# Performance work log

Hardware: AMD Instinct MI355X
Metric: run time of the kernel (lower is better)

## Reference

```python
import jax, jax.numpy as jnp
import numpy as np

S_MUL, V_MUL = 32, 16          # 32x0e + 16x1o
NODE_DIM = S_MUL + 3 * V_MUL   # 80
LATENT = 128
INV_SQRT3 = 1.0 / np.sqrt(3.0)          # wigner 3j (1,1,0) / (0,1,1) / (1,0,1) factor
C_SCALAR = np.float32(1.0 / np.sqrt(48.0))   # path_norm 'element': fan into 0e = 32*1 + 16*1
C_VECTOR = np.float32(np.sqrt(3.0 / 48.0))   # irrep dim 3 / fan 48 for 1o output


def setup_inputs() -> dict:
    rng = np.random.default_rng(0)
    B, n_atoms, radius = 2048, 32, 5.0
    N = B * n_atoms
    # atoms uniform in a 10A cube -> ~300 edges per 32-atom graph at r=5
    pos_g = rng.uniform(0.0, 10.0, size=(B, n_atoms, 3)).astype(np.float32)
    diff = pos_g[:, :, None, :] - pos_g[:, None, :, :]
    d2 = (diff * diff).sum(-1)
    mask = (d2 <= radius * radius) & (d2 > 0.0)   # same predicate as build_radius_graph
    b_idx, i_idx, j_idx = np.nonzero(mask)
    edge_index = np.stack([b_idx * n_atoms + i_idx, b_idx * n_atoms + j_idx]).astype(np.int32)
    pos = pos_g.reshape(N, 3)
    z = rng.integers(0, 100, size=N).astype(np.int32)
    batch = np.repeat(np.arange(B, dtype=np.int32), n_atoms)
    L = 3  # num_layers

    def w(*shape, scale=1.0):
        return jnp.asarray((rng.standard_normal(shape) * scale).astype(np.float32))

    return dict(
        pos=jnp.asarray(pos), z=jnp.asarray(z), batch=jnp.asarray(batch),
        edge_index=jnp.asarray(edge_index), num_graphs=B,
        emb=w(100, S_MUL),                      # nn.Embedding(100, 32) ~ N(0,1)
        W_s2n=w(S_MUL, S_MUL),                  # e3nn Linear 32x0e -> 32x0e path
        W1=w(L, S_MUL, S_MUL),                  # tp path 0e x 0e -> 0e
        W2=w(L, S_MUL, V_MUL),                  # tp path 0e x 1o -> 1o
        W3=w(L, V_MUL, V_MUL),                  # tp path 1o x 0e -> 1o
        W4=w(L, V_MUL, S_MUL),                  # tp path 1o x 1o -> 0e
        Ws=w(L, S_MUL, S_MUL),                  # e3nn Linear scalar block
        Wv=w(L, V_MUL, V_MUL),                  # e3nn Linear vector block
        Wr1=w(NODE_DIM, 256, scale=1.0 / np.sqrt(NODE_DIM)), br1=jnp.zeros((256,), jnp.float32),
        Wr2=w(256, LATENT, scale=1.0 / np.sqrt(256.0)), br2=jnp.zeros((LATENT,), jnp.float32),
    )


def _forward(pos, emb, W_s2n, W1, W2, W3, W4, Ws, Wv, Wr1, br1, Wr2, br2,
             z, batch, edge_index, num_graphs):
    N = pos.shape[0]
    src, dst = edge_index[0], edge_index[1]
    # atom embedding -> node irreps (only 0e->0e path exists; vectors start at 0)
    s = (emb[z] @ W_s2n) * np.float32(1.0 / np.sqrt(S_MUL))   # (N, 32)
    v = jnp.zeros((N, V_MUL, 3), pos.dtype)                   # (N, 16, 3)
    # spherical harmonics, normalize=True, 'component': Y0 = 1, Y1 = sqrt(3) * r_hat
    rij = pos[dst] - pos[src]                                 # (E, 3)
    sh1 = np.float32(np.sqrt(3.0)) * rij / jnp.linalg.norm(rij, axis=-1, keepdims=True)
    for l in range(W1.shape[0]):
        ss, vs = s[src], v[src]                               # gather (E,32), (E,16,3)
        # FullyConnectedTensorProduct(node, sh, node), uvw weights, sh0 == 1
        m_s = C_SCALAR * (jnp.einsum('eu,uw->ew', ss, W1[l])
                          + INV_SQRT3 * jnp.einsum('eui,ei,uw->ew', vs, sh1, W4[l]))
        m_v = (C_VECTOR * INV_SQRT3) * (jnp.einsum('eu,ei,uw->ewi', ss, sh1, W2[l])
                                        + jnp.einsum('eui,uw->ewi', vs, W3[l]))
        a_s = jax.ops.segment_sum(m_s, dst, num_segments=N)   # index_add_ scatter
        a_v = jax.ops.segment_sum(m_v, dst, num_segments=N)
        # e3nn Linear (per-irrep block, 1/sqrt(fan_in)) then relu on FULL feature (as in source)
        h_s = jax.nn.relu((a_s @ Ws[l]) * np.float32(1.0 / np.sqrt(S_MUL)))
        h_v = jax.nn.relu(jnp.einsum('nvi,vw->nwi', a_v, Wv[l]) * np.float32(1.0 / np.sqrt(V_MUL)))
        s, v = s + h_s, v + h_v                               # residual
    x = jnp.concatenate([s, v.reshape(N, V_MUL * 3)], axis=-1)  # (N, 80)
    hg = jax.ops.segment_sum(x, batch, num_segments=num_graphs) # sum-pool per graph
    return jax.nn.relu(hg @ Wr1 + br1) @ Wr2 + br2              # (B, latent)


def reference(pos, emb, W_s2n, W1, W2, W3, W4, Ws, Wv, Wr1, br1, Wr2, br2,
              z, batch, edge_index, num_graphs):
    return _forward(pos, emb, W_s2n, W1, W2, W3, W4, Ws, Wv, Wr1, br1, Wr2, br2,
                    z, batch, edge_index, num_graphs)
```

## Files before the change

### kernel.cpp

```cpp
#include <hip/hip_runtime.h>
#include <math.h>

typedef __attribute__((ext_vector_type(8))) short bf16x8;
typedef __attribute__((ext_vector_type(4))) float f32x4;

#define SQRT3F     1.7320508075688772f
#define SCALE_T    0.17677669529663687f
#define SCALE_M1   0.025515518153991442f
#define SCALE_M2   0.014731391274719739f
#define SCALE_M34  0.036084391824351615f

#define FSTR 40
#define ASTR 72

__device__ __forceinline__ ushort f2bf(float f) {
    union { float f; unsigned u; } v; v.f = f;
    unsigned u = v.u;
    return (ushort)((u + 0x7FFFu + ((u >> 16) & 1u)) >> 16);
}
__device__ __forceinline__ float bf2f(ushort h) {
    union { unsigned u; float f; } v; v.u = ((unsigned)h) << 16;
    return v.f;
}
__device__ __forceinline__ f32x4 mfma(bf16x8 a, bf16x8 b, f32x4 c) {
    return __builtin_amdgcn_mfma_f32_16x16x32_bf16(a, b, c, 0, 0, 0);
}
__device__ __forceinline__ void storeAgg(ushort* AG, f32x4 t, int u0, int n) {
    uint2 u;
    u.x = f2bf(t[0]) | ((unsigned)f2bf(t[1]) << 16);
    u.y = f2bf(t[2]) | ((unsigned)f2bf(t[3]) << 16);
    *(uint2*)&AG[n*ASTR + u0] = u;
}

__global__ void prep_kernel(const float* __restrict__ pos,
                            const float* __restrict__ emb,
                            const float* __restrict__ W_s2n,
                            const float* __restrict__ W1, const float* __restrict__ W2,
                            const float* __restrict__ W3, const float* __restrict__ W4,
                            const float* __restrict__ Ws, const float* __restrict__ Wv,
                            ushort* __restrict__ adjF, ushort* __restrict__ Tbf,
                            ushort* __restrict__ Mbf, int NG)
{
    int idx = blockIdx.x * blockDim.x + threadIdx.x;
    const int NA = NG * 2 * 64;
    if (idx < NA) {
        int g = idx >> 7, r = idx & 127, nt = r >> 6, l = r & 63;
        int nl = nt*16 + (l & 15);
        int k0 = (l >> 4) * 8;
        int ng = g*32 + nl;
        float px = pos[3*ng], py = pos[3*ng+1], pz = pos[3*ng+2];
        ushort o0[8], o1[8], o2[8], o3[8];
        #pragma unroll
        for (int jj = 0; jj < 8; ++jj) {
            int j = g*32 + k0 + jj;
            float dx = __fsub_rn(px, pos[3*j]);
            float dy = __fsub_rn(py, pos[3*j+1]);
            float dz = __fsub_rn(pz, pos[3*j+2]);
            float d2 = __fadd_rn(__fadd_rn(__fmul_rn(dx,dx), __fmul_rn(dy,dy)),
                                 __fmul_rn(dz,dz));
            bool on = (d2 <= 25.0f) && (d2 > 0.0f);
            float rinv = on ? rsqrtf(d2) * SQRT3F : 0.f;
            o0[jj] = on ? f2bf(1.0f) : 0;
            o1[jj] = f2bf(dx * rinv);
            o2[jj] = f2bf(dy * rinv);
            o3[jj] = f2bf(dz * rinv);
        }
        const ushort* srcs[4] = {o0, o1, o2, o3};
        #pragma unroll
        for (int w = 0; w < 4; ++w) {
            const ushort* s = srcs[w];
            uint4 u;
            u.x = s[0] | ((unsigned)s[1] << 16);
            u.y = s[2] | ((unsigned)s[3] << 16);
            u.z = s[4] | ((unsigned)s[5] << 16);
            u.w = s[6] | ((unsigned)s[7] << 16);
            *(uint4*)(adjF + (((size_t)(g*4 + w)*2 + nt)*64 + l)*8) = u;
        }
        return;
    }
    idx -= NA;
    if (idx < 3200) {
        int r = idx >> 5, c = idx & 31;
        float acc = 0.f;
        for (int k = 0; k < 32; ++k) acc += emb[r*32 + k] * W_s2n[k*32 + c];
        Tbf[idx] = f2bf(acc * SCALE_T);
        return;
    }
    idx -= 3200;
    if (idx < 3*48*64) {
        int lyr = idx / 3072, rem = idx % 3072;
        int row = rem >> 6, u = rem & 63;
        float val = 0.f;
        if (row < 32) {
            int w = row;
            if (u < 32) {
                float a = 0.f;
                for (int k = 0; k < 32; ++k)
                    a += W1[lyr*1024 + u*32 + k] * Ws[lyr*1024 + k*32 + w];
                val = a * SCALE_M1;
            } else if (u < 48) {
                int uu = u - 32; float a = 0.f;
                for (int k = 0; k < 32; ++k)
                    a += W4[lyr*512 + uu*32 + k] * Ws[lyr*1024 + k*32 + w];
                val = a * SCALE_M2;
            }
        } else {
            int w = row - 32;
            if (u < 32) {
                float a = 0.f;
                for (int k = 0; k < 16; ++k)
                    a += W2[lyr*512 + u*16 + k] * Wv[lyr*256 + k*16 + w];
                val = a * SCALE_M34;
            } else if (u < 48) {
                int uu = u - 32; float a = 0.f;
                for (int k = 0; k < 16; ++k)
                    a += W3[lyr*256 + uu*16 + k] * Wv[lyr*256 + k*16 + w];
                val = a * SCALE_M34;
            }
        }
        Mbf[lyr*3072 + row*64 + u] = f2bf(val);
    }
}

__global__ __launch_bounds__(256)
void gnn_kernel(const ushort* __restrict__ Tbf, const int* __restrict__ z,
                const ushort* __restrict__ adjF, const ushort* __restrict__ Mbf,
                float* __restrict__ hg, int B)
{
    __shared__ ushort lM[3*48*ASTR];
    __shared__ ushort feat[4][80*FSTR];
    __shared__ ushort agg[4][32*ASTR];

    const int tid = threadIdx.x;
    for (int i = tid; i < 3*48*8; i += 256) {
        int row = i >> 3, u0 = (i & 7) * 8;
        uint4 m = *(const uint4*)(Mbf + row*64 + u0);
        uint2 a; a.x = m.x; a.y = m.y;
        uint2 b; b.x = m.z; b.y = m.w;
        *(uint2*)&lM[row*ASTR + u0]     = a;
        *(uint2*)&lM[row*ASTR + u0 + 4] = b;
    }
    const int wv = tid >> 6, l = tid & 63;
    const int g  = blockIdx.x*4 + wv;
    ushort* F  = feat[wv];
    ushort* AG = agg[wv];

    for (int i = l; i < 32*(ASTR/2); i += 64) ((uint*)AG)[i] = 0;
    for (int i = l; i < 48*(FSTR/2); i += 64) ((uint*)(F + 32*FSTR))[i] = 0;
    {
        int n = l & 31, h = l >> 5;
        int zg = z[g*32 + n];
        uint4 t0 = *(const uint4*)(Tbf + zg*32 + h*16);
        uint4 t1 = *(const uint4*)(Tbf + zg*32 + h*16 + 8);
        unsigned ua[8] = {t0.x, t0.y, t0.z, t0.w, t1.x, t1.y, t1.z, t1.w};
        #pragma unroll
        for (int q = 0; q < 8; ++q) {
            F[(h*16 + 2*q    )*FSTR + n] = (ushort)ua[q];
            F[(h*16 + 2*q + 1)*FSTR + n] = (ushort)(ua[q] >> 16);
        }
    }
    bf16x8 adjf[4][2];
    #pragma unroll
    for (int w = 0; w < 4; ++w)
        #pragma unroll
        for (int nt = 0; nt < 2; ++nt)
            adjf[w][nt] = *(const bf16x8*)(adjF + (((size_t)(g*4 + w)*2 + nt)*64 + l)*8);
    __syncthreads();

    const int ln = l & 15, kq = l >> 4;
    const f32x4 z4 = {0.f, 0.f, 0.f, 0.f};

    for (int lay = 0; lay < 3; ++lay) {
        const ushort* Msl = lM + lay*48*ASTR;
        bf16x8 fs0 = *(const bf16x8*)&F[(     ln)*FSTR + kq*8];
        bf16x8 fs1 = *(const bf16x8*)&F[(16 + ln)*FSTR + kq*8];
        bf16x8 fv0 = *(const bf16x8*)&F[(32 + ln)*FSTR + kq*8];
        bf16x8 fv1 = *(const bf16x8*)&F[(48 + ln)*FSTR + kq*8];
        bf16x8 fv2 = *(const bf16x8*)&F[(64 + ln)*FSTR + kq*8];

        #pragma unroll
        for (int nt = 0; nt < 2; ++nt) {
            f32x4 t;
            t = mfma(fs0, adjf[0][nt], z4);
            storeAgg(AG, t,      kq*4, nt*16 + ln);
            t = mfma(fs1, adjf[0][nt], z4);
            storeAgg(AG, t, 16 + kq*4, nt*16 + ln);
            t = mfma(fv2, adjf[3][nt], z4);
            t = mfma(fv1, adjf[2][nt], t);
            t = mfma(fv0, adjf[1][nt], t);
            storeAgg(AG, t, 32 + kq*4, nt*16 + ln);
        }
        f32x4 hs[2][2] = {{z4, z4}, {z4, z4}};
        #pragma unroll
        for (int kc = 0; kc < 2; ++kc) {
            bf16x8 m0 = *(const bf16x8*)&Msl[(     ln)*ASTR + kc*32 + kq*8];
            bf16x8 m1 = *(const bf16x8*)&Msl[(16 + ln)*ASTR + kc*32 + kq*8];
            #pragma unroll
            for (int nt = 0; nt < 2; ++nt) {
                bf16x8 bg = *(const bf16x8*)&AG[(nt*16 + ln)*ASTR + kc*32 + kq*8];
                hs[0][nt] = mfma(m0, bg, hs[0][nt]);
                hs[1][nt] = mfma(m1, bg, hs[1][nt]);
            }
        }
        #pragma unroll
        for (int mt = 0; mt < 2; ++mt)
            #pragma unroll
            for (int nt = 0; nt < 2; ++nt) {
                int n = nt*16 + ln;
                #pragma unroll
                for (int r = 0; r < 4; ++r) {
                    int c = mt*16 + kq*4 + r;
                    ushort* p = &F[c*FSTR + n];
                    *p = f2bf(bf2f(*p) + fmaxf(hs[mt][nt][r], 0.f));
                }
            }

        #pragma unroll
        for (int i = 0; i < 3; ++i) {
            bf16x8 fvi = (i == 0) ? fv0 : (i == 1) ? fv1 : fv2;
            #pragma unroll
            for (int nt = 0; nt < 2; ++nt) {
                f32x4 t;
                t = mfma(fs0, adjf[1+i][nt], z4);
                storeAgg(AG, t,      kq*4, nt*16 + ln);
                t = mfma(fs1, adjf[1+i][nt], z4);
                storeAgg(AG, t, 16 + kq*4, nt*16 + ln);
                t = mfma(fvi, adjf[0][nt], z4);
                storeAgg(AG, t, 32 + kq*4, nt*16 + ln);
            }
            f32x4 hv[2] = {z4, z4};
            #pragma unroll
            for (int kc = 0; kc < 2; ++kc) {
                bf16x8 mv = *(const bf16x8*)&Msl[(32 + ln)*ASTR + kc*32 + kq*8];
                #pragma unroll
                for (int nt = 0; nt < 2; ++nt) {
                    bf16x8 bg = *(const bf16x8*)&AG[(nt*16 + ln)*ASTR + kc*32 + kq*8];
                    hv[nt] = mfma(mv, bg, hv[nt]);
                }
            }
            #pragma unroll
            for (int nt = 0; nt < 2; ++nt) {
                int n = nt*16 + ln;
                #pragma unroll
                for (int r = 0; r < 4; ++r) {
                    int c = 32 + i*16 + kq*4 + r;
                    ushort* p = &F[c*FSTR + n];
                    *p = f2bf(bf2f(*p) + fmaxf(hv[nt][r], 0.f));
                }
            }
        }
    }

    for (int f = l; f < 80; f += 64) {
        const ushort* row;
        if (f < 32) row = &F[f*FSTR];
        else { int c = f - 32, w = c/3, i = c - 3*w; row = &F[(32 + i*16 + w)*FSTR]; }
        const uint* r32 = (const uint*)row;
        float acc = 0.f;
        #pragma unroll
        for (int q = 0; q < 16; ++q) {
            uint u = r32[q];
            acc += bf2f((ushort)u) + bf2f((ushort)(u >> 16));
        }
        hg[(size_t)g*80 + f] = acc;
    }
}

__launch_bounds__(256)
__global__ void mlp_kernel(const float* __restrict__ hg,
                           const float* __restrict__ Wr1, const float* __restrict__ br1,
                           const float* __restrict__ Wr2, const float* __restrict__ br2,
                           float* __restrict__ out, int B)
{
    __shared__ __align__(16) float h1[4][256];
    __shared__ float red[4][128];
    const int g0 = blockIdx.x * 4;
    const int w = threadIdx.x;

    float acc0 = br1[w];
    float acc1 = acc0, acc2 = acc0, acc3 = acc0;
    #pragma unroll 4
    for (int f = 0; f < 80; ++f) {
        float wv = Wr1[f*256 + w];
        acc0 = fmaf(hg[(size_t)(g0+0)*80 + f], wv, acc0);
        acc1 = fmaf(hg[(size_t)(g0+1)*80 + f], wv, acc1);
        acc2 = fmaf(hg[(size_t)(g0+2)*80 + f], wv, acc2);
        acc3 = fmaf(hg[(size_t)(g0+3)*80 + f], wv, acc3);
    }
    h1[0][w] = fmaxf(acc0, 0.f);
    h1[1][w] = fmaxf(acc1, 0.f);
    h1[2][w] = fmaxf(acc2, 0.f);
    h1[3][w] = fmaxf(acc3, 0.f);
    __syncthreads();

    const int w2 = threadIdx.x & 127, kh = threadIdx.x >> 7;
    const float4* h1v = (const float4*)(&h1[0][0]);
    float s0 = 0.f, s1 = 0.f, s2 = 0.f, s3 = 0.f;
    #pragma unroll 2
    for (int k4 = kh*32; k4 < kh*32 + 32; ++k4) {
        float4 hA = h1v[0*64 + k4];
        float4 hB = h1v[1*64 + k4];
        float4 hC = h1v[2*64 + k4];
        float4 hD = h1v[3*64 + k4];
        int k = k4 * 4;
        float m0 = Wr2[(size_t)(k+0)*128 + w2];
        float m1 = Wr2[(size_t)(k+1)*128 + w2];
        float m2 = Wr2[(size_t)(k+2)*128 + w2];
        float m3 = Wr2[(size_t)(k+3)*128 + w2];
        s0 = fmaf(hA.x,m0, fmaf(hA.y,m1, fmaf(hA.z,m2, fmaf(hA.w,m3, s0))));
        s1 = fmaf(hB.x,m0, fmaf(hB.y,m1, fmaf(hB.z,m2, fmaf(hB.w,m3, s1))));
        s2 = fmaf(hC.x,m0, fmaf(hC.y,m1, fmaf(hC.z,m2, fmaf(hC.w,m3, s2))));
        s3 = fmaf(hD.x,m0, fmaf(hD.y,m1, fmaf(hD.z,m2, fmaf(hD.w,m3, s3))));
    }
    if (kh) {
        red[0][w2] = s0; red[1][w2] = s1; red[2][w2] = s2; red[3][w2] = s3;
    }
    __syncthreads();
    if (!kh) {
        float b = br2[w2];
        out[(size_t)(g0+0)*128 + w2] = s0 + red[0][w2] + b;
        out[(size_t)(g0+1)*128 + w2] = s1 + red[1][w2] + b;
        out[(size_t)(g0+2)*128 + w2] = s2 + red[2][w2] + b;
        out[(size_t)(g0+3)*128 + w2] = s3 + red[3][w2] + b;
    }
}

extern "C" void kernel_launch(void* const* d_in, const int* in_sizes, int n_in,
                              void* d_out, int out_size, void* d_ws, size_t ws_size,
                              hipStream_t stream)
{
    const float* pos   = (const float*)d_in[0];
    const int*   z     = (const int*)d_in[1];
    const float* emb   = (const float*)d_in[5];
    const float* W_s2n = (const float*)d_in[6];
    const float* W1    = (const float*)d_in[7];
    const float* W2    = (const float*)d_in[8];
    const float* W3    = (const float*)d_in[9];
    const float* W4    = (const float*)d_in[10];
    const float* Ws    = (const float*)d_in[11];
    const float* Wv    = (const float*)d_in[12];
    const float* Wr1   = (const float*)d_in[13];
    const float* br1   = (const float*)d_in[14];
    const float* Wr2   = (const float*)d_in[15];
    const float* br2   = (const float*)d_in[16];
    float* out = (float*)d_out;

    const int B = out_size / 128;
    const int NG = B;

    char* p = (char*)d_ws;
    ushort* adjF = (ushort*)p;  p += (size_t)NG * 4 * 2 * 64 * 8 * 2;
    ushort* Tbf  = (ushort*)p;  p += ((3200*2 + 15) & ~15);
    ushort* Mbf  = (ushort*)p;  p += ((3*48*64*2 + 15) & ~15);
    float*  hg   = (float*)p;   p += (size_t)B * 80 * 4;

    const int prep_total = NG*2*64 + 3200 + 3*48*64;
    prep_kernel<<<(prep_total + 255) / 256, 256, 0, stream>>>(
        pos, emb, W_s2n, W1, W2, W3, W4, Ws, Wv, adjF, Tbf, Mbf, NG);

    gnn_kernel<<<B / 4, 256, 0, stream>>>(Tbf, z, adjF, Mbf, hg, B);

    mlp_kernel<<<B / 4, 256, 0, stream>>>(hg, Wr1, br1, Wr2, br2, out, B);
}
```

Before: 125.9 us.

## Fuse prep, GNN and MLP kernels into a single launch

Merges the three kernels into one. Each block now builds the folded weight matrices, embeddings and adjacency fragments in registers or shared memory itself, and runs the readout MLP on its four graphs from shared memory. This removes two launches and the global round trips for adjF, Tbf, Mbf and hg. In exchange every block recomputes the 3x48x64 weight products and the embedding matmuls, which is redundant work across 512 blocks, and shared memory use grows to about 66KB.

```diff
diff --git a/kernel.cpp b/kernel.cpp
--- a/kernel.cpp
+++ b/kernel.cpp
@@ -32,62 +32,27 @@
     *(uint2*)&AG[n*ASTR + u0] = u;
 }
 
-__global__ void prep_kernel(const float* __restrict__ pos,
-                            const float* __restrict__ emb,
-                            const float* __restrict__ W_s2n,
-                            const float* __restrict__ W1, const float* __restrict__ W2,
-                            const float* __restrict__ W3, const float* __restrict__ W4,
-                            const float* __restrict__ Ws, const float* __restrict__ Wv,
-                            ushort* __restrict__ adjF, ushort* __restrict__ Tbf,
-                            ushort* __restrict__ Mbf, int NG)
+__global__ __launch_bounds__(256)
+void gnn_kernel(const float* __restrict__ pos, const int* __restrict__ z,
+                const float* __restrict__ emb, const float* __restrict__ W_s2n,
+                const float* __restrict__ W1, const float* __restrict__ W2,
+                const float* __restrict__ W3, const float* __restrict__ W4,
+                const float* __restrict__ Ws, const float* __restrict__ Wv,
+                const float* __restrict__ Wr1, const float* __restrict__ br1,
+                const float* __restrict__ Wr2, const float* __restrict__ br2,
+                float* __restrict__ out, int B)
 {
-    int idx = blockIdx.x * blockDim.x + threadIdx.x;
-    const int NA = NG * 2 * 64;
-    if (idx < NA) {
-        int g = idx >> 7, r = idx & 127, nt = r >> 6, l = r & 63;
-        int nl = nt*16 + (l & 15);
-        int k0 = (l >> 4) * 8;
-        int ng = g*32 + nl;
-        float px = pos[3*ng], py = pos[3*ng+1], pz = pos[3*ng+2];
-        ushort o0[8], o1[8], o2[8], o3[8];
-        #pragma unroll
-        for (int jj = 0; jj < 8; ++jj) {
-            int j = g*32 + k0 + jj;
-            float dx = __fsub_rn(px, pos[3*j]);
-            float dy = __fsub_rn(py, pos[3*j+1]);
-            float dz = __fsub_rn(pz, pos[3*j+2]);
-            float d2 = __fadd_rn(__fadd_rn(__fmul_rn(dx,dx), __fmul_rn(dy,dy)),
-                                 __fmul_rn(dz,dz));
-            bool on = (d2 <= 25.0f) && (d2 > 0.0f);
-            float rinv = on ? rsqrtf(d2) * SQRT3F : 0.f;
-            o0[jj] = on ? f2bf(1.0f) : 0;
-            o1[jj] = f2bf(dx * rinv);
-            o2[jj] = f2bf(dy * rinv);
-            o3[jj] = f2bf(dz * rinv);
-        }
-        const ushort* srcs[4] = {o0, o1, o2, o3};
-        #pragma unroll
-        for (int w = 0; w < 4; ++w) {
-            const ushort* s = srcs[w];
-            uint4 u;
-            u.x = s[0] | ((unsigned)s[1] << 16);
-            u.y = s[2] | ((unsigned)s[3] << 16);
-            u.z = s[4] | ((unsigned)s[5] << 16);
-            u.w = s[6] | ((unsigned)s[7] << 16);
-            *(uint4*)(adjF + (((size_t)(g*4 + w)*2 + nt)*64 + l)*8) = u;
-        }
-        return;
-    }
-    idx -= NA;
-    if (idx < 3200) {
-        int r = idx >> 5, c = idx & 31;
-        float acc = 0.f;
-        for (int k = 0; k < 32; ++k) acc += emb[r*32 + k] * W_s2n[k*32 + c];
-        Tbf[idx] = f2bf(acc * SCALE_T);
-        return;
-    }
-    idx -= 3200;
-    if (idx < 3*48*64) {
+    __shared__ __align__(16) char smem[66048];
+    ushort* lM    = (ushort*)smem;
+    ushort* featA = (ushort*)(smem + 20736);
+    ushort* aggA  = (ushort*)(smem + 46336);
+    float*  hgl   = (float*)(smem + 64768);
+    float*  h1    = (float*)aggA;
+    float*  red   = ((float*)aggA) + 1024;
+
+    const int tid = threadIdx.x;
+
+    for (int idx = tid; idx < 3*48*64; idx += 256) {
         int lyr = idx / 3072, rem = idx % 3072;
         int row = rem >> 6, u = rem & 63;
         float val = 0.f;
@@ -118,56 +83,59 @@
                 val = a * SCALE_M34;
             }
         }
-        Mbf[lyr*3072 + row*64 + u] = f2bf(val);
-    }
-}
-
-__global__ __launch_bounds__(256)
-void gnn_kernel(const ushort* __restrict__ Tbf, const int* __restrict__ z,
-                const ushort* __restrict__ adjF, const ushort* __restrict__ Mbf,
-                float* __restrict__ hg, int B)
-{
-    __shared__ ushort lM[3*48*ASTR];
-    __shared__ ushort feat[4][80*FSTR];
-    __shared__ ushort agg[4][32*ASTR];
-
-    const int tid = threadIdx.x;
-    for (int i = tid; i < 3*48*8; i += 256) {
-        int row = i >> 3, u0 = (i & 7) * 8;
-        uint4 m = *(const uint4*)(Mbf + row*64 + u0);
-        uint2 a; a.x = m.x; a.y = m.y;
-        uint2 b; b.x = m.z; b.y = m.w;
-        *(uint2*)&lM[row*ASTR + u0]     = a;
-        *(uint2*)&lM[row*ASTR + u0 + 4] = b;
-    }
+        lM[lyr*48*ASTR + row*ASTR + u] = f2bf(val);
+    }
+
     const int wv = tid >> 6, l = tid & 63;
     const int g  = blockIdx.x*4 + wv;
-    ushort* F  = feat[wv];
-    ushort* AG = agg[wv];
+    ushort* F  = featA + wv*80*FSTR;
+    ushort* AG = aggA  + wv*32*ASTR;
 
     for (int i = l; i < 32*(ASTR/2); i += 64) ((uint*)AG)[i] = 0;
     for (int i = l; i < 48*(FSTR/2); i += 64) ((uint*)(F + 32*FSTR))[i] = 0;
+
     {
         int n = l & 31, h = l >> 5;
         int zg = z[g*32 + n];
-        uint4 t0 = *(const uint4*)(Tbf + zg*32 + h*16);
-        uint4 t1 = *(const uint4*)(Tbf + zg*32 + h*16 + 8);
-        unsigned ua[8] = {t0.x, t0.y, t0.z, t0.w, t1.x, t1.y, t1.z, t1.w};
-        #pragma unroll
-        for (int q = 0; q < 8; ++q) {
-            F[(h*16 + 2*q    )*FSTR + n] = (ushort)ua[q];
-            F[(h*16 + 2*q + 1)*FSTR + n] = (ushort)(ua[q] >> 16);
-        }
-    }
+        const float* er = emb + (size_t)zg*32;
+        for (int cc = 0; cc < 16; ++cc) {
+            int c = h*16 + cc;
+            float acc = 0.f;
+            for (int k = 0; k < 32; ++k) acc += er[k] * W_s2n[k*32 + c];
+            F[c*FSTR + n] = f2bf(acc * SCALE_T);
+        }
+    }
+
+    const int ln = l & 15, kq = l >> 4;
     bf16x8 adjf[4][2];
-    #pragma unroll
-    for (int w = 0; w < 4; ++w)
-        #pragma unroll
-        for (int nt = 0; nt < 2; ++nt)
-            adjf[w][nt] = *(const bf16x8*)(adjF + (((size_t)(g*4 + w)*2 + nt)*64 + l)*8);
+    {
+        const int k0 = kq*8;
+        #pragma unroll
+        for (int nt = 0; nt < 2; ++nt) {
+            int ng = g*32 + nt*16 + ln;
+            float px = pos[3*ng], py = pos[3*ng+1], pz = pos[3*ng+2];
+            union { bf16x8 v; ushort s[8]; } o[4];
+            #pragma unroll
+            for (int jj = 0; jj < 8; ++jj) {
+                int j = g*32 + k0 + jj;
+                float dx = __fsub_rn(px, pos[3*j]);
+                float dy = __fsub_rn(py, pos[3*j+1]);
+                float dz = __fsub_rn(pz, pos[3*j+2]);
+                float d2 = __fadd_rn(__fadd_rn(__fmul_rn(dx,dx), __fmul_rn(dy,dy)),
+                                     __fmul_rn(dz,dz));
+                bool on = (d2 <= 25.0f) && (d2 > 0.0f);
+                float rinv = on ? rsqrtf(d2) * SQRT3F : 0.f;
+                o[0].s[jj] = on ? (ushort)0x3F80 : (ushort)0;
+                o[1].s[jj] = f2bf(dx * rinv);
+                o[2].s[jj] = f2bf(dy * rinv);
+                o[3].s[jj] = f2bf(dz * rinv);
+            }
+            #pragma unroll
+            for (int w = 0; w < 4; ++w) adjf[w][nt] = o[w].v;
+        }
+    }
     __syncthreads();
 
-    const int ln = l & 15, kq = l >> 4;
     const f32x4 z4 = {0.f, 0.f, 0.f, 0.f};
 
     for (int lay = 0; lay < 3; ++lay) {
@@ -262,66 +230,61 @@
             uint u = r32[q];
             acc += bf2f((ushort)u) + bf2f((ushort)(u >> 16));
         }
-        hg[(size_t)g*80 + f] = acc;
-    }
-}
-
-__launch_bounds__(256)
-__global__ void mlp_kernel(const float* __restrict__ hg,
-                           const float* __restrict__ Wr1, const float* __restrict__ br1,
-                           const float* __restrict__ Wr2, const float* __restrict__ br2,
-                           float* __restrict__ out, int B)
-{
-    __shared__ __align__(16) float h1[4][256];
-    __shared__ float red[4][128];
-    const int g0 = blockIdx.x * 4;
-    const int w = threadIdx.x;
-
-    float acc0 = br1[w];
-    float acc1 = acc0, acc2 = acc0, acc3 = acc0;
-    #pragma unroll 4
-    for (int f = 0; f < 80; ++f) {
-        float wv = Wr1[f*256 + w];
-        acc0 = fmaf(hg[(size_t)(g0+0)*80 + f], wv, acc0);
-        acc1 = fmaf(hg[(size_t)(g0+1)*80 + f], wv, acc1);
-        acc2 = fmaf(hg[(size_t)(g0+2)*80 + f], wv, acc2);
-        acc3 = fmaf(hg[(size_t)(g0+3)*80 + f], wv, acc3);
-    }
-    h1[0][w] = fmaxf(acc0, 0.f);
-    h1[1][w] = fmaxf(acc1, 0.f);
-    h1[2][w] = fmaxf(acc2, 0.f);
-    h1[3][w] = fmaxf(acc3, 0.f);
+        hgl[wv*80 + f] = acc;
+    }
     __syncthreads();
 
-    const int w2 = threadIdx.x & 127, kh = threadIdx.x >> 7;
-    const float4* h1v = (const float4*)(&h1[0][0]);
-    float s0 = 0.f, s1 = 0.f, s2 = 0.f, s3 = 0.f;
-    #pragma unroll 2
-    for (int k4 = kh*32; k4 < kh*32 + 32; ++k4) {
-        float4 hA = h1v[0*64 + k4];
-        float4 hB = h1v[1*64 + k4];
-        float4 hC = h1v[2*64 + k4];
-        float4 hD = h1v[3*64 + k4];
-        int k = k4 * 4;
-        float m0 = Wr2[(size_t)(k+0)*128 + w2];
-        float m1 = Wr2[(size_t)(k+1)*128 + w2];
-        float m2 = Wr2[(size_t)(k+2)*128 + w2];
-        float m3 = Wr2[(size_t)(k+3)*128 + w2];
-        s0 = fmaf(hA.x,m0, fmaf(hA.y,m1, fmaf(hA.z,m2, fmaf(hA.w,m3, s0))));
-        s1 = fmaf(hB.x,m0, fmaf(hB.y,m1, fmaf(hB.z,m2, fmaf(hB.w,m3, s1))));
-        s2 = fmaf(hC.x,m0, fmaf(hC.y,m1, fmaf(hC.z,m2, fmaf(hC.w,m3, s2))));
-        s3 = fmaf(hD.x,m0, fmaf(hD.y,m1, fmaf(hD.z,m2, fmaf(hD.w,m3, s3))));
-    }
-    if (kh) {
-        red[0][w2] = s0; red[1][w2] = s1; red[2][w2] = s2; red[3][w2] = s3;
+    {
+        const int w = tid;
+        float acc0 = br1[w];
+        float acc1 = acc0, acc2 = acc0, acc3 = acc0;
+        #pragma unroll 4
+        for (int f = 0; f < 80; ++f) {
+            float wvv = Wr1[f*256 + w];
+            acc0 = fmaf(hgl[0*80 + f], wvv, acc0);
+            acc1 = fmaf(hgl[1*80 + f], wvv, acc1);
+            acc2 = fmaf(hgl[2*80 + f], wvv, acc2);
+            acc3 = fmaf(hgl[3*80 + f], wvv, acc3);
+        }
+        h1[0*256 + w] = fmaxf(acc0, 0.f);
+        h1[1*256 + w] = fmaxf(acc1, 0.f);
+        h1[2*256 + w] = fmaxf(acc2, 0.f);
+        h1[3*256 + w] = fmaxf(acc3, 0.f);
     }
     __syncthreads();
-    if (!kh) {
-        float b = br2[w2];
-        out[(size_t)(g0+0)*128 + w2] = s0 + red[0][w2] + b;
-        out[(size_t)(g0+1)*128 + w2] = s1 + red[1][w2] + b;
-        out[(size_t)(g0+2)*128 + w2] = s2 + red[2][w2] + b;
-        out[(size_t)(g0+3)*128 + w2] = s3 + red[3][w2] + b;
+    {
+        const int g0 = blockIdx.x * 4;
+        const int w2 = tid & 127, kh = tid >> 7;
+        const float4* h1v = (const float4*)h1;
+        float s0 = 0.f, s1 = 0.f, s2 = 0.f, s3 = 0.f;
+        #pragma unroll 2
+        for (int k4 = kh*32; k4 < kh*32 + 32; ++k4) {
+            float4 hA = h1v[0*64 + k4];
+            float4 hB = h1v[1*64 + k4];
+            float4 hC = h1v[2*64 + k4];
+            float4 hD = h1v[3*64 + k4];
+            int k = k4 * 4;
+            float m0 = Wr2[(size_t)(k+0)*128 + w2];
+            float m1 = Wr2[(size_t)(k+1)*128 + w2];
+            float m2 = Wr2[(size_t)(k+2)*128 + w2];
+            float m3 = Wr2[(size_t)(k+3)*128 + w2];
+            s0 = fmaf(hA.x,m0, fmaf(hA.y,m1, fmaf(hA.z,m2, fmaf(hA.w,m3, s0))));
+            s1 = fmaf(hB.x,m0, fmaf(hB.y,m1, fmaf(hB.z,m2, fmaf(hB.w,m3, s1))));
+            s2 = fmaf(hC.x,m0, fmaf(hC.y,m1, fmaf(hC.z,m2, fmaf(hC.w,m3, s2))));
+            s3 = fmaf(hD.x,m0, fmaf(hD.y,m1, fmaf(hD.z,m2, fmaf(hD.w,m3, s3))));
+        }
+        if (kh) {
+            red[0*128 + w2] = s0; red[1*128 + w2] = s1;
+            red[2*128 + w2] = s2; red[3*128 + w2] = s3;
+        }
+        __syncthreads();
+        if (!kh) {
+            float b = br2[w2];
+            out[(size_t)(g0+0)*128 + w2] = s0 + red[0*128 + w2] + b;
+            out[(size_t)(g0+1)*128 + w2] = s1 + red[1*128 + w2] + b;
+            out[(size_t)(g0+2)*128 + w2] = s2 + red[2*128 + w2] + b;
+            out[(size_t)(g0+3)*128 + w2] = s3 + red[3*128 + w2] + b;
+        }
     }
 }
 
@@ -346,19 +309,7 @@
     float* out = (float*)d_out;
 
     const int B = out_size / 128;
-    const int NG = B;
-
-    char* p = (char*)d_ws;
-    ushort* adjF = (ushort*)p;  p += (size_t)NG * 4 * 2 * 64 * 8 * 2;
-    ushort* Tbf  = (ushort*)p;  p += ((3200*2 + 15) & ~15);
-    ushort* Mbf  = (ushort*)p;  p += ((3*48*64*2 + 15) & ~15);
-    float*  hg   = (float*)p;   p += (size_t)B * 80 * 4;
-
-    const int prep_total = NG*2*64 + 3200 + 3*48*64;
-    prep_kernel<<<(prep_total + 255) / 256, 256, 0, stream>>>(
-        pos, emb, W_s2n, W1, W2, W3, W4, Ws, Wv, adjF, Tbf, Mbf, NG);
-
-    gnn_kernel<<<B / 4, 256, 0, stream>>>(Tbf, z, adjF, Mbf, hg, B);
-
-    mlp_kernel<<<B / 4, 256, 0, stream>>>(hg, Wr1, br1, Wr2, br2, out, B);
-}
+
+    gnn_kernel<<<B / 4, 256, 0, stream>>>(pos, z, emb, W_s2n, W1, W2, W3, W4,
+                                          Ws, Wv, Wr1, br1, Wr2, br2, out, B);
+}
```

After: 200.0 us. +58.9%, slower.
